# Kernel optimization log

Hardware: AMD Instinct MI355X
Metric: run time of the kernel (lower is better)

## Reference

```python
import jax, jax.numpy as jnp
import numpy as np

N_NODES = 100000
N_EDGES = 3200000


def gcn_conv(x, W, b, row, col, n):
    # PyG GCNConv: add self-loops, symmetric normalization D^-1/2 (A+I) D^-1/2 (X W) + b
    xw = x @ W  # [N, out]
    loops = jnp.arange(n)
    row2 = jnp.concatenate([row, loops])
    col2 = jnp.concatenate([col, loops])
    deg = jax.ops.segment_sum(jnp.ones_like(col2, dtype=xw.dtype), col2, num_segments=n)
    dinv = jnp.where(deg > 0, jax.lax.rsqrt(deg), 0.0)
    norm = dinv[row2] * dinv[col2]  # [E+N]
    msg = xw[row2] * norm[:, None]  # gather + scale
    out = jax.ops.segment_sum(msg, col2, num_segments=n)  # scatter-add to targets
    return out + b


def setup_inputs() -> dict:
    key = jax.random.key(0)
    ks = jax.random.split(key, 9)
    x = jax.random.normal(ks[0], (N_NODES, 2), dtype=jnp.float32)
    edge_index = jax.random.randint(ks[1], (2, N_EDGES), 0, N_NODES, dtype=jnp.int64)
    edge_attr = jax.random.normal(ks[2], (N_EDGES, 1), dtype=jnp.float32)
    # params (glorot-ish scale)
    W1 = jax.random.normal(ks[3], (2, 16), dtype=jnp.float32) * (1.0 / np.sqrt(2))
    b1 = jnp.zeros((16,), dtype=jnp.float32)
    We = jax.random.normal(ks[4], (33, 4), dtype=jnp.float32) * (1.0 / np.sqrt(33))
    be = jnp.zeros((4,), dtype=jnp.float32)
    W2 = jax.random.normal(ks[5], (16, 2), dtype=jnp.float32) * (1.0 / np.sqrt(16))
    b2 = jnp.zeros((2,), dtype=jnp.float32)
    return {"x": x, "edge_index": edge_index, "edge_attr": edge_attr,
            "W1": W1, "b1": b1, "We": We, "be": be, "W2": W2, "b2": b2}


def reference(x, edge_index, edge_attr, W1, b1, We, be, W2, b2):
    row, col = edge_index[0], edge_index[1]
    n = x.shape[0]
    h = gcn_conv(x, W1, b1, row, col, n)  # [N, 16]
    # edge update: gather src/dst features, concat with edge_attr, Linear+ReLU
    e_in = jnp.concatenate([h[row], edge_attr, h[col]], axis=1)  # [E, 33]
    e_out = jax.nn.relu(e_in @ We + be)  # [E, 4]
    out_x = gcn_conv(h, W2, b2, row, col, n)  # [N, 2]
    return jax.nn.log_softmax(out_x, axis=1), jax.nn.log_softmax(e_out, axis=1)
```

## Files before the change

kernel.cpp:

```cpp
#include <hip/hip_runtime.h>


#define BLK 256
#define CH 8192
#define BSH 7
#define BSZ 128
#define NBMAX 1024
#define S1 262144.0f
#define S2 65536.0f
#define BIAS 8388608

__global__ void k_hist(const int* __restrict__ col, int* __restrict__ gcount,
                       int E, int NB) {
    __shared__ int hist[NBMAX];
    int t = threadIdx.x;
    for (int b = t; b < NB; b += BLK) hist[b] = 0;
    __syncthreads();
    int e0 = blockIdx.x * CH;
    int cnt = min(CH, E - e0);
    for (int k = t; k < cnt; k += BLK)
        atomicAdd(&hist[col[e0 + k] >> BSH], 1);
    __syncthreads();
    for (int b = t; b < NB; b += BLK) {
        int h = hist[b];
        if (h) atomicAdd(&gcount[b], h);
    }
}

__global__ void k_scan(const int* __restrict__ gcount, int* __restrict__ gbase,
                       int* __restrict__ gcursor, int NB) {
    __shared__ int sa[NBMAX], sb[NBMAX];
    int t = threadIdx.x;
    for (int i = t; i < NBMAX; i += BLK) sa[i] = (i < NB) ? gcount[i] : 0;
    __syncthreads();
    int *src = sa, *dst = sb;
    for (int off = 1; off < NBMAX; off <<= 1) {
        for (int i = t; i < NBMAX; i += BLK)
            dst[i] = src[i] + ((i >= off) ? src[i - off] : 0);
        __syncthreads();
        int* tmp = src; src = dst; dst = tmp;
    }
    for (int i = t; i < NB; i += BLK) {
        int ex = src[i] - gcount[i];
        gbase[i] = ex;
        gcursor[i] = ex;
    }
    if (t == 0) gbase[NB] = src[NB - 1];
}

__global__ void k_part(const int* __restrict__ row, const int* __restrict__ col,
                       int* __restrict__ gcursor, unsigned* __restrict__ part,
                       int E, int NB) {
    __shared__ int sa[NBMAX], sb[NBMAX];
    __shared__ int hist[NBMAX], lstart[NBMAX], lcur[NBMAX], gb[NBMAX];
    __shared__ unsigned sbuf[CH];
    __shared__ unsigned short bid[CH];
    int t = threadIdx.x;
    int e0 = blockIdx.x * CH;
    int cnt = min(CH, E - e0);
    for (int b = t; b < NB; b += BLK) hist[b] = 0;
    __syncthreads();
    for (int k = t; k < cnt; k += BLK)
        atomicAdd(&hist[col[e0 + k] >> BSH], 1);
    __syncthreads();
    for (int i = t; i < NBMAX; i += BLK) sa[i] = (i < NB) ? hist[i] : 0;
    __syncthreads();
    int *src = sa, *dst = sb;
    for (int off = 1; off < NBMAX; off <<= 1) {
        for (int i = t; i < NBMAX; i += BLK)
            dst[i] = src[i] + ((i >= off) ? src[i - off] : 0);
        __syncthreads();
        int* tmp = src; src = dst; dst = tmp;
    }
    for (int i = t; i < NB; i += BLK) {
        int h = hist[i];
        int ex = src[i] - h;
        lstart[i] = ex;
        lcur[i] = ex;
        gb[i] = h ? atomicAdd(&gcursor[i], h) : 0;
    }
    __syncthreads();
    for (int k = t; k < cnt; k += BLK) {
        int e = e0 + k;
        int c = col[e], r = row[e];
        int b = c >> BSH;
        int off = atomicAdd(&lcur[b], 1);
        sbuf[off] = ((unsigned)r << BSH) | (unsigned)(c & (BSZ - 1));
        bid[off] = (unsigned short)b;
    }
    __syncthreads();
    for (int j = t; j < cnt; j += BLK) {
        int b = bid[j];
        part[gb[b] + (j - lstart[b])] = sbuf[j];
    }
}

__global__ void k_nodeA(const unsigned* __restrict__ part, const int* __restrict__ gbase,
                        const float2* __restrict__ x2, float* __restrict__ dinv,
                        int* __restrict__ degi, int2* __restrict__ pi, int N) {
    __shared__ int cnt[BSZ];
    int t = threadIdx.x;
    if (t < BSZ) cnt[t] = 0;
    __syncthreads();
    int b = blockIdx.x;
    int j0 = gbase[b], j1 = gbase[b + 1];
    for (int j = j0 + t; j < j1; j += BLK)
        atomicAdd(&cnt[part[j] & (BSZ - 1)], 1);
    __syncthreads();
    if (t < BSZ) {
        int node = (b << BSH) + t;
        if (node < N) {
            int dg = cnt[t];
            degi[node] = dg;
            float d = rsqrtf((float)(dg + 1));
            dinv[node] = d;
            float2 xv = x2[node];
            pi[node] = make_int2(__float2int_rn(xv.x * d * S1),
                                 __float2int_rn(xv.y * d * S1));
        }
    }
}

__global__ void k_nodeB(const unsigned* __restrict__ part, const int* __restrict__ gbase,
                        const float* __restrict__ dinv, const int* __restrict__ degi,
                        const int2* __restrict__ pi,
                        const float* __restrict__ W1, const float* __restrict__ b1,
                        const float* __restrict__ W2, const float* __restrict__ We,
                        const float* __restrict__ be,
                        float4* __restrict__ U, float4* __restrict__ V,
                        int2* __restrict__ qi, int N) {
    __shared__ unsigned long long acc[BSZ];
    __shared__ float sW1[32], sb1[16], sW2[32], sWr[64], sWc[64], sbe[4];
    int t = threadIdx.x;
    if (t < BSZ) acc[t] = 0ull;
    if (t < 32) sW1[t] = W1[t];
    else if (t < 64) sW2[t - 32] = W2[t - 32];
    else if (t < 80) sb1[t - 64] = b1[t - 64];
    else if (t < 144) sWr[t - 80] = We[t - 80];
    else if (t < 208) sWc[t - 144] = We[68 + (t - 144)];
    else if (t < 212) sbe[t - 208] = be[t - 208];
    __syncthreads();
    int b = blockIdx.x;
    int j0 = gbase[b], j1 = gbase[b + 1];
    for (int j = j0 + t; j < j1; j += BLK) {
        unsigned w = part[j];
        int2 pv = pi[w >> BSH];
        int l = (int)(w & (BSZ - 1));
        unsigned long long val =
            ((unsigned long long)(unsigned)pv.x << 32) | (unsigned)(pv.y + BIAS);
        atomicAdd(&acc[l], val);
    }
    __syncthreads();
    if (t < BSZ) {
        int node = (b << BSH) + t;
        if (node < N) {
            unsigned long long a = acc[t];
            int sx = (int)(unsigned)(a >> 32);
            long long sy = (long long)(unsigned)(a & 0xffffffffull)
                         - (long long)degi[node] * BIAS;
            int2 ps = pi[node];
            float d = dinv[node];
            float ax = (float)(ps.x + (long long)sx) * (1.0f / S1);
            float ay = (float)(ps.y + sy) * (1.0f / S1);
            float s0 = d * ax, s1 = d * ay;
            float u0 = sbe[0], u1 = sbe[1], u2 = sbe[2], u3 = sbe[3];
            float v0 = 0.f, v1 = 0.f, v2 = 0.f, v3 = 0.f;
            float w0 = 0.f, w1 = 0.f;
            #pragma unroll
            for (int jj = 0; jj < 16; jj++) {
                float hj = fmaf(s0, sW1[jj], fmaf(s1, sW1[16 + jj], sb1[jj]));
                u0 = fmaf(hj, sWr[4 * jj + 0], u0);
                u1 = fmaf(hj, sWr[4 * jj + 1], u1);
                u2 = fmaf(hj, sWr[4 * jj + 2], u2);
                u3 = fmaf(hj, sWr[4 * jj + 3], u3);
                v0 = fmaf(hj, sWc[4 * jj + 0], v0);
                v1 = fmaf(hj, sWc[4 * jj + 1], v1);
                v2 = fmaf(hj, sWc[4 * jj + 2], v2);
                v3 = fmaf(hj, sWc[4 * jj + 3], v3);
                w0 = fmaf(hj, sW2[2 * jj], w0);
                w1 = fmaf(hj, sW2[2 * jj + 1], w1);
            }
            U[node] = make_float4(u0, u1, u2, u3);
            V[node] = make_float4(v0, v1, v2, v3);
            float qx = w0 * d, qy = w1 * d;
            qi[node] = make_int2(__float2int_rn(qx * S2), __float2int_rn(qy * S2));
        }
    }
}

__global__ void k_edge(const int* __restrict__ row, const int* __restrict__ col,
                       const float* __restrict__ ea, const float4* __restrict__ U,
                       const float4* __restrict__ V, const float* __restrict__ We,
                       float4* __restrict__ eout, int E) {
    __shared__ float sW16[4];
    int t = threadIdx.x;
    if (t < 4) sW16[t] = We[64 + t];
    __syncthreads();
    int e = blockIdx.x * BLK + t;
    if (e < E) {
        float4 u = U[row[e]];
        float4 v = V[col[e]];
        float av = ea[e];
        float a0 = u.x + fmaf(av, sW16[0], v.x);
        float a1 = u.y + fmaf(av, sW16[1], v.y);
        float a2 = u.z + fmaf(av, sW16[2], v.z);
        float a3 = u.w + fmaf(av, sW16[3], v.w);
        a0 = fmaxf(a0, 0.f); a1 = fmaxf(a1, 0.f);
        a2 = fmaxf(a2, 0.f); a3 = fmaxf(a3, 0.f);
        float m = fmaxf(fmaxf(a0, a1), fmaxf(a2, a3));
        float s = expf(a0 - m) + expf(a1 - m) + expf(a2 - m) + expf(a3 - m);
        float l = m + logf(s);
        eout[e] = make_float4(a0 - l, a1 - l, a2 - l, a3 - l);
    }
}

__global__ void k_nodeC(const unsigned* __restrict__ part, const int* __restrict__ gbase,
                        const float* __restrict__ dinv, const int* __restrict__ degi,
                        const int2* __restrict__ qi,
                        const float* __restrict__ b2, float2* __restrict__ outn, int N) {
    __shared__ unsigned long long acc[BSZ];
    int t = threadIdx.x;
    if (t < BSZ) acc[t] = 0ull;
    __syncthreads();
    int b = blockIdx.x;
    int j0 = gbase[b], j1 = gbase[b + 1];
    for (int j = j0 + t; j < j1; j += BLK) {
        unsigned w = part[j];
        int2 qv = qi[w >> BSH];
        int l = (int)(w & (BSZ - 1));
        unsigned long long val =
            ((unsigned long long)(unsigned)qv.x << 32) | (unsigned)(qv.y + BIAS);
        atomicAdd(&acc[l], val);
    }
    __syncthreads();
    if (t < BSZ) {
        int node = (b << BSH) + t;
        if (node < N) {
            unsigned long long a = acc[t];
            int sx = (int)(unsigned)(a >> 32);
            long long sy = (long long)(unsigned)(a & 0xffffffffull)
                         - (long long)degi[node] * BIAS;
            int2 qs = qi[node];
            float d = dinv[node];
            float bx = (float)(qs.x + (long long)sx) * (1.0f / S2);
            float by = (float)(qs.y + sy) * (1.0f / S2);
            float o0 = fmaf(d, bx, b2[0]);
            float o1 = fmaf(d, by, b2[1]);
            float m = fmaxf(o0, o1);
            float l2 = m + logf(expf(o0 - m) + expf(o1 - m));
            outn[node] = make_float2(o0 - l2, o1 - l2);
        }
    }
}

extern "C" void kernel_launch(void* const* d_in, const int* in_sizes, int n_in,
                              void* d_out, int out_size, void* d_ws, size_t ws_size,
                              hipStream_t stream) {
    const float* x  = (const float*)d_in[0];
    const int*   ei = (const int*)d_in[1];
    const float* ea = (const float*)d_in[2];
    const float* W1 = (const float*)d_in[3];
    const float* b1 = (const float*)d_in[4];
    const float* We = (const float*)d_in[5];
    const float* be = (const float*)d_in[6];
    const float* W2 = (const float*)d_in[7];
    const float* b2 = (const float*)d_in[8];

    const int N = in_sizes[0] / 2;
    const int E = in_sizes[2];
    const int* row = ei;
    const int* col = ei + E;
    const int NB  = (N + BSZ - 1) >> BSH;
    const int NCH = (E + CH - 1) / CH;

    float2* out_nodes = (float2*)d_out;
    float4* out_edges = (float4*)((float*)d_out + 2 * (size_t)N);

    char* ws = (char*)d_ws;
    int*      gcount  = (int*)     (ws + 0);
    int*      gbase   = (int*)     (ws + 4096);
    int*      gcursor = (int*)     (ws + 12288);
    float*    dinv    = (float*)   (ws + 16384);
    int*      degi    = (int*)     (ws + 416384);
    int2*     pi      = (int2*)    (ws + 816384);
    int2*     qi      = (int2*)    (ws + 1616384);
    float4*   U       = (float4*)  (ws + 2416384);
    float4*   V       = (float4*)  (ws + 4016384);
    unsigned* part    = (unsigned*)(ws + 5616384);

    hipMemsetAsync(gcount, 0, NBMAX * sizeof(int), stream);
    k_hist <<<NCH, BLK, 0, stream>>>(col, gcount, E, NB);
    k_scan <<<1,   BLK, 0, stream>>>(gcount, gbase, gcursor, NB);
    k_part <<<NCH, BLK, 0, stream>>>(row, col, gcursor, part, E, NB);
    k_nodeA<<<NB,  BLK, 0, stream>>>(part, gbase, (const float2*)x, dinv, degi, pi, N);
    k_nodeB<<<NB,  BLK, 0, stream>>>(part, gbase, dinv, degi, pi, W1, b1, W2, We, be, U, V, qi, N);
    k_edge <<<(E + BLK - 1) / BLK, BLK, 0, stream>>>(row, col, ea, U, V, We, out_edges, E);
    k_nodeC<<<NB,  BLK, 0, stream>>>(part, gbase, dinv, degi, qi, b2, out_nodes, N);
}
```

Measured before the change: 249.0 us.

## Reuse per-chunk histograms in partition and unroll gather loops by four

The histogram kernel now saves each chunk's per-bucket counts to a workspace array. The partition kernel reads those counts instead of recomputing the histogram and running a shared-memory scan. It also drops the local shared-memory staging and scatters each edge straight to global memory through a shared atomic cursor per bucket, which removes large LDS use and raises occupancy but gives less coalesced writes. Separately, the node aggregation loops are unrolled by four so several part and pi/qi loads are in flight before the shared atomics.

```diff
diff --git a/kernel.cpp b/kernel.cpp
--- a/kernel.cpp
+++ b/kernel.cpp
@@ -6,12 +6,13 @@
 #define BSH 7
 #define BSZ 128
 #define NBMAX 1024
+#define NBP 1024
 #define S1 262144.0f
 #define S2 65536.0f
 #define BIAS 8388608
 
 __global__ void k_hist(const int* __restrict__ col, int* __restrict__ gcount,
-                       int E, int NB) {
+                       int* __restrict__ ccnt, int E, int NB) {
     __shared__ int hist[NBMAX];
     int t = threadIdx.x;
     for (int b = t; b < NB; b += BLK) hist[b] = 0;
@@ -21,8 +22,10 @@
     for (int k = t; k < cnt; k += BLK)
         atomicAdd(&hist[col[e0 + k] >> BSH], 1);
     __syncthreads();
+    int* crow = ccnt + (size_t)blockIdx.x * NBP;
     for (int b = t; b < NB; b += BLK) {
         int h = hist[b];
+        crow[b] = h;
         if (h) atomicAdd(&gcount[b], h);
     }
 }
@@ -49,49 +52,24 @@
 }
 
 __global__ void k_part(const int* __restrict__ row, const int* __restrict__ col,
-                       int* __restrict__ gcursor, unsigned* __restrict__ part,
-                       int E, int NB) {
-    __shared__ int sa[NBMAX], sb[NBMAX];
-    __shared__ int hist[NBMAX], lstart[NBMAX], lcur[NBMAX], gb[NBMAX];
-    __shared__ unsigned sbuf[CH];
-    __shared__ unsigned short bid[CH];
+                       const int* __restrict__ ccnt, int* __restrict__ gcursor,
+                       unsigned* __restrict__ part, int E, int NB) {
+    __shared__ int gb[NBMAX];
     int t = threadIdx.x;
     int e0 = blockIdx.x * CH;
     int cnt = min(CH, E - e0);
-    for (int b = t; b < NB; b += BLK) hist[b] = 0;
-    __syncthreads();
-    for (int k = t; k < cnt; k += BLK)
-        atomicAdd(&hist[col[e0 + k] >> BSH], 1);
-    __syncthreads();
-    for (int i = t; i < NBMAX; i += BLK) sa[i] = (i < NB) ? hist[i] : 0;
-    __syncthreads();
-    int *src = sa, *dst = sb;
-    for (int off = 1; off < NBMAX; off <<= 1) {
-        for (int i = t; i < NBMAX; i += BLK)
-            dst[i] = src[i] + ((i >= off) ? src[i - off] : 0);
-        __syncthreads();
-        int* tmp = src; src = dst; dst = tmp;
-    }
-    for (int i = t; i < NB; i += BLK) {
-        int h = hist[i];
-        int ex = src[i] - h;
-        lstart[i] = ex;
-        lcur[i] = ex;
-        gb[i] = h ? atomicAdd(&gcursor[i], h) : 0;
+    const int* crow = ccnt + (size_t)blockIdx.x * NBP;
+    for (int b = t; b < NB; b += BLK) {
+        int h = crow[b];
+        gb[b] = h ? atomicAdd(&gcursor[b], h) : 0;
     }
     __syncthreads();
     for (int k = t; k < cnt; k += BLK) {
         int e = e0 + k;
-        int c = col[e], r = row[e];
+        int c = col[e];
         int b = c >> BSH;
-        int off = atomicAdd(&lcur[b], 1);
-        sbuf[off] = ((unsigned)r << BSH) | (unsigned)(c & (BSZ - 1));
-        bid[off] = (unsigned short)b;
-    }
-    __syncthreads();
-    for (int j = t; j < cnt; j += BLK) {
-        int b = bid[j];
-        part[gb[b] + (j - lstart[b])] = sbuf[j];
+        int off = atomicAdd(&gb[b], 1);
+        part[off] = ((unsigned)row[e] << BSH) | (unsigned)(c & (BSZ - 1));
     }
 }
 
@@ -104,7 +82,16 @@
     __syncthreads();
     int b = blockIdx.x;
     int j0 = gbase[b], j1 = gbase[b + 1];
-    for (int j = j0 + t; j < j1; j += BLK)
+    int j = j0 + t;
+    for (; j + 3 * BLK < j1; j += 4 * BLK) {
+        unsigned w0 = part[j], w1 = part[j + BLK];
+        unsigned w2 = part[j + 2 * BLK], w3 = part[j + 3 * BLK];
+        atomicAdd(&cnt[w0 & (BSZ - 1)], 1);
+        atomicAdd(&cnt[w1 & (BSZ - 1)], 1);
+        atomicAdd(&cnt[w2 & (BSZ - 1)], 1);
+        atomicAdd(&cnt[w3 & (BSZ - 1)], 1);
+    }
+    for (; j < j1; j += BLK)
         atomicAdd(&cnt[part[j] & (BSZ - 1)], 1);
     __syncthreads();
     if (t < BSZ) {
@@ -121,6 +108,10 @@
     }
 }
 
+__device__ __forceinline__ unsigned long long pack64(int2 v) {
+    return ((unsigned long long)(unsigned)v.x << 32) | (unsigned)(v.y + BIAS);
+}
+
 __global__ void k_nodeB(const unsigned* __restrict__ part, const int* __restrict__ gbase,
                         const float* __restrict__ dinv, const int* __restrict__ degi,
                         const int2* __restrict__ pi,
@@ -142,13 +133,20 @@
     __syncthreads();
     int b = blockIdx.x;
     int j0 = gbase[b], j1 = gbase[b + 1];
-    for (int j = j0 + t; j < j1; j += BLK) {
+    int j = j0 + t;
+    for (; j + 3 * BLK < j1; j += 4 * BLK) {
+        unsigned w0 = part[j], w1 = part[j + BLK];
+        unsigned w2 = part[j + 2 * BLK], w3 = part[j + 3 * BLK];
+        int2 p0 = pi[w0 >> BSH], p1 = pi[w1 >> BSH];
+        int2 p2 = pi[w2 >> BSH], p3 = pi[w3 >> BSH];
+        atomicAdd(&acc[w0 & (BSZ - 1)], pack64(p0));
+        atomicAdd(&acc[w1 & (BSZ - 1)], pack64(p1));
+        atomicAdd(&acc[w2 & (BSZ - 1)], pack64(p2));
+        atomicAdd(&acc[w3 & (BSZ - 1)], pack64(p3));
+    }
+    for (; j < j1; j += BLK) {
         unsigned w = part[j];
-        int2 pv = pi[w >> BSH];
-        int l = (int)(w & (BSZ - 1));
-        unsigned long long val =
-            ((unsigned long long)(unsigned)pv.x << 32) | (unsigned)(pv.y + BIAS);
-        atomicAdd(&acc[l], val);
+        atomicAdd(&acc[w & (BSZ - 1)], pack64(pi[w >> BSH]));
     }
     __syncthreads();
     if (t < BSZ) {
@@ -224,13 +222,20 @@
     __syncthreads();
     int b = blockIdx.x;
     int j0 = gbase[b], j1 = gbase[b + 1];
-    for (int j = j0 + t; j < j1; j += BLK) {
+    int j = j0 + t;
+    for (; j + 3 * BLK < j1; j += 4 * BLK) {
+        unsigned w0 = part[j], w1 = part[j + BLK];
+        unsigned w2 = part[j + 2 * BLK], w3 = part[j + 3 * BLK];
+        int2 q0 = qi[w0 >> BSH], q1 = qi[w1 >> BSH];
+        int2 q2 = qi[w2 >> BSH], q3 = qi[w3 >> BSH];
+        atomicAdd(&acc[w0 & (BSZ - 1)], pack64(q0));
+        atomicAdd(&acc[w1 & (BSZ - 1)], pack64(q1));
+        atomicAdd(&acc[w2 & (BSZ - 1)], pack64(q2));
+        atomicAdd(&acc[w3 & (BSZ - 1)], pack64(q3));
+    }
+    for (; j < j1; j += BLK) {
         unsigned w = part[j];
-        int2 qv = qi[w >> BSH];
-        int l = (int)(w & (BSZ - 1));
-        unsigned long long val =
-            ((unsigned long long)(unsigned)qv.x << 32) | (unsigned)(qv.y + BIAS);
-        atomicAdd(&acc[l], val);
+        atomicAdd(&acc[w & (BSZ - 1)], pack64(qi[w >> BSH]));
     }
     __syncthreads();
     if (t < BSZ) {
@@ -287,11 +292,12 @@
     float4*   U       = (float4*)  (ws + 2416384);
     float4*   V       = (float4*)  (ws + 4016384);
     unsigned* part    = (unsigned*)(ws + 5616384);
+    int*      ccnt    = (int*)     (ws + 18416384);
 
     hipMemsetAsync(gcount, 0, NBMAX * sizeof(int), stream);
-    k_hist <<<NCH, BLK, 0, stream>>>(col, gcount, E, NB);
+    k_hist <<<NCH, BLK, 0, stream>>>(col, gcount, ccnt, E, NB);
     k_scan <<<1,   BLK, 0, stream>>>(gcount, gbase, gcursor, NB);
-    k_part <<<NCH, BLK, 0, stream>>>(row, col, gcursor, part, E, NB);
+    k_part <<<NCH, BLK, 0, stream>>>(row, col, ccnt, gcursor, part, E, NB);
     k_nodeA<<<NB,  BLK, 0, stream>>>(part, gbase, (const float2*)x, dinv, degi, pi, N);
     k_nodeB<<<NB,  BLK, 0, stream>>>(part, gbase, dinv, degi, pi, W1, b1, W2, We, be, U, V, qi, N);
     k_edge <<<(E + BLK - 1) / BLK, BLK, 0, stream>>>(row, col, ea, U, V, We, out_edges, E);
```

Measured after the change: 268.7 us. +7.9%, slower.
